# Performance work log

Measured on AMD Instinct MI355X. Metric: run time of the kernel, lower is better.

## Reference

```python
import jax, jax.numpy as jnp
import numpy as np

Z_DIM = 64
K = 2048
N = 32768


def setup_inputs() -> dict:
    key = jax.random.key(0)
    k1, k2 = jax.random.split(key)
    x = jax.random.normal(k1, (N, Z_DIM), dtype=jnp.float32)
    # init.normal_(locs, std=sqrt(z_dim))
    locs = jax.random.normal(k2, (K, Z_DIM), dtype=jnp.float32) * np.sqrt(Z_DIM)
    logits = jnp.zeros((K,), dtype=jnp.float32)  # maxent buffer
    return {"x": x, "locs": locs, "logits": logits}


def reference(x, locs, logits):
    d = x.shape[-1]
    var = jnp.float32(d)  # scale = sqrt(z_dim) -> variance = z_dim
    # squared distances [N, K] via cdist expansion (avoids [N,K,d] intermediate)
    sq = (
        jnp.sum(x * x, axis=-1, keepdims=True)
        + jnp.sum(locs * locs, axis=-1)[None, :]
        - 2.0 * (x @ locs.T)
    )
    # Independent Normal log prob summed over z_dim
    log_norm_const = d * (0.5 * jnp.log(2.0 * jnp.pi) + 0.5 * jnp.log(var))
    comp_log_prob = -0.5 * sq / var - log_norm_const  # [N, K]
    mix_logits = jax.nn.log_softmax(logits)  # Categorical normalizes logits
    wlp = comp_log_prob + mix_logits  # weighted_log_prob, [N, K]
    log_prob = jax.nn.logsumexp(wlp, axis=-1)  # [N]
    modes = jnp.argmax(wlp, axis=-1)  # assign_modes, [N]
    quantized = locs[modes]  # hard_quantize, [N, z_dim]
    return log_prob, quantized
```

## Files before the change

### kernel.cpp

```cpp
#include <hip/hip_runtime.h>
#include <math.h>

#define N_SAMP 32768
#define K_COMP 2048
#define ZD 64
#define LNC 191.896324792608546f
#define LN2F 0.69314718055994531f
#define INV_LN2 1.44269504088896340f
#define S2C 0.02254211001388974f

#define TILES_TOT 128
#define TPS 4
#define STAGES (TILES_TOT / TPS)

typedef __attribute__((ext_vector_type(8))) short short8;
typedef __attribute__((ext_vector_type(4))) float v4f;

#if __has_builtin(__builtin_amdgcn_exp2f)
#define EXP2(x) __builtin_amdgcn_exp2f(x)
#else
#define EXP2(x) exp2f(x)
#endif

typedef const __attribute__((address_space(1))) unsigned int* gas_t;
typedef __attribute__((address_space(3))) unsigned int* las_t;
__device__ inline void gload_lds16(const void* g, void* l) {
    __builtin_amdgcn_global_load_lds((gas_t)g, (las_t)l, 16, 0, 0);
}

__device__ inline unsigned short f2bf(float f) {
    unsigned int u = __float_as_uint(f);
    u += 0x7fffu + ((u >> 16) & 1u);
    return (unsigned short)(u >> 16);
}
__device__ inline float bf2f(unsigned short h) {
    return __uint_as_float(((unsigned int)h) << 16);
}

__global__ __launch_bounds__(256) void prep_kernel(
    const float* __restrict__ locs, const float* __restrict__ logits,
    float* __restrict__ ck2, float* __restrict__ lse_out,
    char* __restrict__ lf) {
    if (blockIdx.x < 32) {
        int gid = blockIdx.x * 256 + threadIdx.x;
        int T = gid >> 6;
        int l = gid & 63;
        int n = l & 15, q = l >> 4;
        int k = T * 16 + n;

        const float* src = locs + (size_t)k * ZD + q * 8;
        float4 u0 = *(const float4*)(src);
        float4 u1 = *(const float4*)(src + 4);
        float4 u2 = *(const float4*)(src + 32);
        float4 u3 = *(const float4*)(src + 36);
        float a[8] = {u0.x, u0.y, u0.z, u0.w, u1.x, u1.y, u1.z, u1.w};
        float b[8] = {u2.x, u2.y, u2.z, u2.w, u3.x, u3.y, u3.z, u3.w};

        short8 h0, h1, l0, l1;
        float sq = 0.f;
#pragma unroll
        for (int j = 0; j < 8; ++j) {
            unsigned short ha = f2bf(a[j]);
            h0[j] = (short)ha; l0[j] = (short)f2bf(a[j] - bf2f(ha));
            unsigned short hb = f2bf(b[j]);
            h1[j] = (short)hb; l1[j] = (short)f2bf(b[j] - bf2f(hb));
            sq = fmaf(a[j], a[j], sq);
            sq = fmaf(b[j], b[j], sq);
        }
        char* dst = lf + (size_t)T * 4096 + l * 16;
        *(short8*)(dst)        = h0;
        *(short8*)(dst + 1024) = h1;
        *(short8*)(dst + 2048) = l0;
        *(short8*)(dst + 3072) = l1;

        sq += __shfl_xor(sq, 16);
        sq += __shfl_xor(sq, 32);
        if (q == 0) ck2[k] = (logits[k] - sq * (1.0f / 128.0f)) * INV_LN2;
    } else {
        __shared__ float red[4];
        int tid = threadIdx.x;
        int wv = tid >> 6, ln = tid & 63;
        float lm = -INFINITY;
        for (int i = tid; i < K_COMP; i += 256) lm = fmaxf(lm, logits[i]);
#pragma unroll
        for (int d = 1; d < 64; d <<= 1) lm = fmaxf(lm, __shfl_xor(lm, d));
        if (ln == 0) red[wv] = lm;
        __syncthreads();
        float M = fmaxf(fmaxf(red[0], red[1]), fmaxf(red[2], red[3]));
        float ls = 0.f;
        for (int i = tid; i < K_COMP; i += 256) ls += __expf(logits[i] - M);
#pragma unroll
        for (int d = 1; d < 64; d <<= 1) ls += __shfl_xor(ls, d);
        __syncthreads();
        if (ln == 0) red[wv] = ls;
        __syncthreads();
        if (tid == 0) *lse_out = M + __logf(red[0] + red[1] + red[2] + red[3]);
    }
}

__global__ __launch_bounds__(256, 2) void mix_kernel(
    const float* __restrict__ x, const float* __restrict__ locs,
    const char* __restrict__ lf, const float* __restrict__ ck2,
    const float* __restrict__ lse_ptr, float* __restrict__ out) {

    __shared__ char buf[2][TPS * 4096];
    __shared__ int amax_sh[64];

    const int tid  = threadIdx.x;
    const int lane = tid & 63;
    const int wv   = __builtin_amdgcn_readfirstlane(tid >> 6);
    const int n    = lane & 15;
    const int quad = lane >> 4;
    const int sbase = blockIdx.x * 64;
    const int srow  = sbase + wv * 16 + n;

    short8 bh0, bh1, bl0, bl1;
    float xs;
    {
        const float* xp = x + (size_t)srow * ZD + quad * 8;
        float4 u0 = *(const float4*)(xp);
        float4 u1 = *(const float4*)(xp + 4);
        float4 u2 = *(const float4*)(xp + 32);
        float4 u3 = *(const float4*)(xp + 36);
        float a[8] = {u0.x, u0.y, u0.z, u0.w, u1.x, u1.y, u1.z, u1.w};
        float b[8] = {u2.x, u2.y, u2.z, u2.w, u3.x, u3.y, u3.z, u3.w};
        float p = 0.f;
#pragma unroll
        for (int j = 0; j < 8; ++j) {
            unsigned short h;
            h = f2bf(a[j]); bh0[j] = (short)h; bl0[j] = (short)f2bf(a[j] - bf2f(h));
            h = f2bf(b[j]); bh1[j] = (short)h; bl1[j] = (short)f2bf(b[j] - bf2f(h));
            p = fmaf(a[j], a[j], p);
            p = fmaf(b[j], b[j], p);
        }
        p += __shfl_xor(p, 16);
        p += __shfl_xor(p, 32);
        xs = p;
    }

    const char* gsrc0 = lf + (size_t)wv * 4096 + lane * 16;
    char* ldst0 = &buf[0][wv * 4096];

#define DMA(S, b) do {                                                   \
    const char* _g = gsrc0 + (size_t)(S) * (TPS * 4096);                 \
    char* _l = ldst0 + (b) * (TPS * 4096);                               \
    gload_lds16(_g, _l);                                                 \
    gload_lds16(_g + 1024, _l + 1024);                                   \
    gload_lds16(_g + 2048, _l + 2048);                                   \
    gload_lds16(_g + 3072, _l + 3072);                                   \
} while (0)

    float mm = -1e30f, s0 = 0.f, s1 = 0.f;
    int ai = 0;

#define EPI(acc, fcv, kb) do {                                                 \
    float w0 = fmaf((acc).x, S2C, (fcv).x);                                    \
    float w1 = fmaf((acc).y, S2C, (fcv).y);                                    \
    float w2 = fmaf((acc).z, S2C, (fcv).z);                                    \
    float w3 = fmaf((acc).w, S2C, (fcv).w);                                    \
    s0 += EXP2(w0) + EXP2(w1);                                                 \
    s1 += EXP2(w2) + EXP2(w3);                                                 \
    float t01 = fmaxf(w0, w1); int i01 = (w1 > w0) ? ((kb) + 1) : ((kb) + 0);  \
    float t23 = fmaxf(w2, w3); int i23 = (w3 > w2) ? ((kb) + 3) : ((kb) + 2);  \
    float tt2 = fmaxf(t01, t23); int it = (t23 > t01) ? i23 : i01;             \
    ai = (tt2 > mm) ? it : ai;                                                 \
    mm = fmaxf(mm, tt2);                                                       \
} while (0)

    DMA(0, 0);
    __syncthreads();

    for (int S = 0; S < STAGES; ++S) {
        const int b = S & 1;
        if (S + 1 < STAGES) DMA(S + 1, b ^ 1);

        const float* ckS = ck2 + S * (TPS * 16) + quad * 4;
        float4 fc0 = *(const float4*)(ckS);
        float4 fc1 = *(const float4*)(ckS + 16);
        float4 fc2 = *(const float4*)(ckS + 32);
        float4 fc3 = *(const float4*)(ckS + 48);

        const char* base = &buf[b][lane * 16];
        const int kb0 = S * (TPS * 16) + quad * 4;

#pragma unroll
        for (int j = 0; j < TPS; j += 2) {
            const char* p0 = base + j * 4096;
            const char* p1 = base + (j + 1) * 4096;
            short8 a00 = *(const short8*)(p0);
            short8 a01 = *(const short8*)(p0 + 1024);
            short8 a02 = *(const short8*)(p0 + 2048);
            short8 a03 = *(const short8*)(p0 + 3072);
            short8 a10 = *(const short8*)(p1);
            short8 a11 = *(const short8*)(p1 + 1024);
            short8 a12 = *(const short8*)(p1 + 2048);
            short8 a13 = *(const short8*)(p1 + 3072);

            v4f ca = {0.f, 0.f, 0.f, 0.f};
            v4f cb = {0.f, 0.f, 0.f, 0.f};
            ca = __builtin_amdgcn_mfma_f32_16x16x32_bf16(a00, bh0, ca, 0, 0, 0);
            cb = __builtin_amdgcn_mfma_f32_16x16x32_bf16(a10, bh0, cb, 0, 0, 0);
            ca = __builtin_amdgcn_mfma_f32_16x16x32_bf16(a01, bh1, ca, 0, 0, 0);
            cb = __builtin_amdgcn_mfma_f32_16x16x32_bf16(a11, bh1, cb, 0, 0, 0);
            ca = __builtin_amdgcn_mfma_f32_16x16x32_bf16(a00, bl0, ca, 0, 0, 0);
            cb = __builtin_amdgcn_mfma_f32_16x16x32_bf16(a10, bl0, cb, 0, 0, 0);
            ca = __builtin_amdgcn_mfma_f32_16x16x32_bf16(a01, bl1, ca, 0, 0, 0);
            cb = __builtin_amdgcn_mfma_f32_16x16x32_bf16(a11, bl1, cb, 0, 0, 0);
            ca = __builtin_amdgcn_mfma_f32_16x16x32_bf16(a02, bh0, ca, 0, 0, 0);
            cb = __builtin_amdgcn_mfma_f32_16x16x32_bf16(a12, bh0, cb, 0, 0, 0);
            ca = __builtin_amdgcn_mfma_f32_16x16x32_bf16(a03, bh1, ca, 0, 0, 0);
            cb = __builtin_amdgcn_mfma_f32_16x16x32_bf16(a13, bh1, cb, 0, 0, 0);

            if (j == 0) { EPI(ca, fc0, kb0 + 0 * 16); EPI(cb, fc1, kb0 + 1 * 16); }
            else        { EPI(ca, fc2, kb0 + 2 * 16); EPI(cb, fc3, kb0 + 3 * 16); }
        }
        __syncthreads();
    }

    float sum = s0 + s1;
#pragma unroll
    for (int d = 16; d <= 32; d <<= 1) {
        sum += __shfl_xor(sum, d);
        float om = __shfl_xor(mm, d);
        int   oa = __shfl_xor(ai, d);
        ai = (om > mm || (om == mm && oa < ai)) ? oa : ai;
        mm = fmaxf(mm, om);
    }

    if (quad == 0) {
        float bias = -xs * (1.0f / 128.0f) - LNC;
        out[srow] = fmaf(__log2f(sum), LN2F, bias - lse_ptr[0]);
        amax_sh[wv * 16 + n] = ai;
    }
    __syncthreads();

    const float4* lq = (const float4*)locs;
    float4* oq = (float4*)(out + N_SAMP + (size_t)sbase * ZD);
#pragma unroll
    for (int i = tid; i < 64 * (ZD / 4); i += 256) {
        int r = i >> 4, c = i & 15;
        oq[i] = lq[(size_t)amax_sh[r] * (ZD / 4) + c];
    }
#undef DMA
#undef EPI
}

extern "C" void kernel_launch(void* const* d_in, const int* in_sizes, int n_in,
                              void* d_out, int out_size, void* d_ws, size_t ws_size,
                              hipStream_t stream) {
    const float* x      = (const float*)d_in[0];
    const float* locs   = (const float*)d_in[1];
    const float* logits = (const float*)d_in[2];
    float* out = (float*)d_out;

    float* ck2 = (float*)d_ws;
    float* lse = ck2 + K_COMP;
    char*  lf  = (char*)d_ws + 16384;

    prep_kernel<<<33, 256, 0, stream>>>(locs, logits, ck2, lse, lf);
    mix_kernel<<<N_SAMP / 64, 256, 0, stream>>>(x, locs, lf, ck2, lse, out);
}
```

Before: 100.4 us.

## Drop low-bf16 locs split, track top-3 candidates and rescore exactly in fp32

The locs operand is now kept only as a single bf16 value, which removes the locs-low terms and cuts the MFMAs per 16-component tile from six to four. It also halves the LDS/global traffic per tile, and the stage size doubles to 8 tiles. Because the lower-precision scores can mis-order near-ties, each row tracks its top-3 groups of four components, and after the loop those 12 candidates are rescored with exact fp32 dot products to choose the argmax. The logsumexp now also uses the reduced-precision dot product, which could loosen accuracy, and the extra top-3 bookkeeping adds work to the inner epilogue.

```diff
diff --git a/kernel.cpp b/kernel.cpp
--- a/kernel.cpp
+++ b/kernel.cpp
@@ -10,8 +10,9 @@
 #define S2C 0.02254211001388974f
 
 #define TILES_TOT 128
-#define TPS 4
+#define TPS 8
 #define STAGES (TILES_TOT / TPS)
+#define STAGE_B (TPS * 2048)
 
 typedef __attribute__((ext_vector_type(8))) short short8;
 typedef __attribute__((ext_vector_type(4))) float v4f;
@@ -36,46 +37,39 @@
 __device__ inline float bf2f(unsigned short h) {
     return __uint_as_float(((unsigned int)h) << 16);
 }
+__device__ inline float med3f(float x, float y, float z) {
+    return fmaxf(fminf(x, y), fminf(fmaxf(x, y), z));
+}
 
 __global__ __launch_bounds__(256) void prep_kernel(
     const float* __restrict__ locs, const float* __restrict__ logits,
     float* __restrict__ ck2, float* __restrict__ lse_out,
     char* __restrict__ lf) {
-    if (blockIdx.x < 32) {
+    if (blockIdx.x < 64) {
         int gid = blockIdx.x * 256 + threadIdx.x;
-        int T = gid >> 6;
-        int l = gid & 63;
-        int n = l & 15, q = l >> 4;
-        int k = T * 16 + n;
-
-        const float* src = locs + (size_t)k * ZD + q * 8;
+        int k = gid >> 3;
+        int dc = gid & 7;
+        int T = k >> 4, n = k & 15;
+
+        const float* src = locs + (size_t)k * ZD + dc * 8;
         float4 u0 = *(const float4*)(src);
         float4 u1 = *(const float4*)(src + 4);
-        float4 u2 = *(const float4*)(src + 32);
-        float4 u3 = *(const float4*)(src + 36);
         float a[8] = {u0.x, u0.y, u0.z, u0.w, u1.x, u1.y, u1.z, u1.w};
-        float b[8] = {u2.x, u2.y, u2.z, u2.w, u3.x, u3.y, u3.z, u3.w};
-
-        short8 h0, h1, l0, l1;
+
+        short8 h;
         float sq = 0.f;
 #pragma unroll
         for (int j = 0; j < 8; ++j) {
-            unsigned short ha = f2bf(a[j]);
-            h0[j] = (short)ha; l0[j] = (short)f2bf(a[j] - bf2f(ha));
-            unsigned short hb = f2bf(b[j]);
-            h1[j] = (short)hb; l1[j] = (short)f2bf(b[j] - bf2f(hb));
+            h[j] = (short)f2bf(a[j]);
             sq = fmaf(a[j], a[j], sq);
-            sq = fmaf(b[j], b[j], sq);
-        }
-        char* dst = lf + (size_t)T * 4096 + l * 16;
-        *(short8*)(dst)        = h0;
-        *(short8*)(dst + 1024) = h1;
-        *(short8*)(dst + 2048) = l0;
-        *(short8*)(dst + 3072) = l1;
-
-        sq += __shfl_xor(sq, 16);
-        sq += __shfl_xor(sq, 32);
-        if (q == 0) ck2[k] = (logits[k] - sq * (1.0f / 128.0f)) * INV_LN2;
+        }
+        *(short8*)(lf + (size_t)T * 2048 + (dc >> 2) * 1024 +
+                   ((size_t)(n + 16 * (dc & 3))) * 16) = h;
+
+        sq += __shfl_xor(sq, 1);
+        sq += __shfl_xor(sq, 2);
+        sq += __shfl_xor(sq, 4);
+        if (dc == 0) ck2[k] = (logits[k] - sq * (1.0f / 128.0f)) * INV_LN2;
     } else {
         __shared__ float red[4];
         int tid = threadIdx.x;
@@ -103,7 +97,8 @@
     const char* __restrict__ lf, const float* __restrict__ ck2,
     const float* __restrict__ lse_ptr, float* __restrict__ out) {
 
-    __shared__ char buf[2][TPS * 4096];
+    __shared__ char buf[2][STAGE_B];
+    __shared__ int cb1[64], cb2[64], cb3[64];
     __shared__ int amax_sh[64];
 
     const int tid  = threadIdx.x;
@@ -142,30 +137,17 @@
     char* ldst0 = &buf[0][wv * 4096];
 
 #define DMA(S, b) do {                                                   \
-    const char* _g = gsrc0 + (size_t)(S) * (TPS * 4096);                 \
-    char* _l = ldst0 + (b) * (TPS * 4096);                               \
+    const char* _g = gsrc0 + (size_t)(S) * STAGE_B;                      \
+    char* _l = ldst0 + (b) * STAGE_B;                                    \
     gload_lds16(_g, _l);                                                 \
     gload_lds16(_g + 1024, _l + 1024);                                   \
     gload_lds16(_g + 2048, _l + 2048);                                   \
     gload_lds16(_g + 3072, _l + 3072);                                   \
 } while (0)
 
-    float mm = -1e30f, s0 = 0.f, s1 = 0.f;
-    int ai = 0;
-
-#define EPI(acc, fcv, kb) do {                                                 \
-    float w0 = fmaf((acc).x, S2C, (fcv).x);                                    \
-    float w1 = fmaf((acc).y, S2C, (fcv).y);                                    \
-    float w2 = fmaf((acc).z, S2C, (fcv).z);                                    \
-    float w3 = fmaf((acc).w, S2C, (fcv).w);                                    \
-    s0 += EXP2(w0) + EXP2(w1);                                                 \
-    s1 += EXP2(w2) + EXP2(w3);                                                 \
-    float t01 = fmaxf(w0, w1); int i01 = (w1 > w0) ? ((kb) + 1) : ((kb) + 0);  \
-    float t23 = fmaxf(w2, w3); int i23 = (w3 > w2) ? ((kb) + 3) : ((kb) + 2);  \
-    float tt2 = fmaxf(t01, t23); int it = (t23 > t01) ? i23 : i01;             \
-    ai = (tt2 > mm) ? it : ai;                                                 \
-    mm = fmaxf(mm, tt2);                                                       \
-} while (0)
+    float m1 = -1e30f, m2 = -1e30f, m3 = -1e30f;
+    int i1 = 0, i2 = 0, i3 = 0;
+    float s0 = 0.f, s1 = 0.f;
 
     DMA(0, 0);
     __syncthreads();
@@ -175,44 +157,42 @@
         if (S + 1 < STAGES) DMA(S + 1, b ^ 1);
 
         const float* ckS = ck2 + S * (TPS * 16) + quad * 4;
-        float4 fc0 = *(const float4*)(ckS);
-        float4 fc1 = *(const float4*)(ckS + 16);
-        float4 fc2 = *(const float4*)(ckS + 32);
-        float4 fc3 = *(const float4*)(ckS + 48);
-
         const char* base = &buf[b][lane * 16];
         const int kb0 = S * (TPS * 16) + quad * 4;
 
 #pragma unroll
-        for (int j = 0; j < TPS; j += 2) {
-            const char* p0 = base + j * 4096;
-            const char* p1 = base + (j + 1) * 4096;
-            short8 a00 = *(const short8*)(p0);
-            short8 a01 = *(const short8*)(p0 + 1024);
-            short8 a02 = *(const short8*)(p0 + 2048);
-            short8 a03 = *(const short8*)(p0 + 3072);
-            short8 a10 = *(const short8*)(p1);
-            short8 a11 = *(const short8*)(p1 + 1024);
-            short8 a12 = *(const short8*)(p1 + 2048);
-            short8 a13 = *(const short8*)(p1 + 3072);
-
-            v4f ca = {0.f, 0.f, 0.f, 0.f};
-            v4f cb = {0.f, 0.f, 0.f, 0.f};
-            ca = __builtin_amdgcn_mfma_f32_16x16x32_bf16(a00, bh0, ca, 0, 0, 0);
-            cb = __builtin_amdgcn_mfma_f32_16x16x32_bf16(a10, bh0, cb, 0, 0, 0);
-            ca = __builtin_amdgcn_mfma_f32_16x16x32_bf16(a01, bh1, ca, 0, 0, 0);
-            cb = __builtin_amdgcn_mfma_f32_16x16x32_bf16(a11, bh1, cb, 0, 0, 0);
-            ca = __builtin_amdgcn_mfma_f32_16x16x32_bf16(a00, bl0, ca, 0, 0, 0);
-            cb = __builtin_amdgcn_mfma_f32_16x16x32_bf16(a10, bl0, cb, 0, 0, 0);
-            ca = __builtin_amdgcn_mfma_f32_16x16x32_bf16(a01, bl1, ca, 0, 0, 0);
-            cb = __builtin_amdgcn_mfma_f32_16x16x32_bf16(a11, bl1, cb, 0, 0, 0);
-            ca = __builtin_amdgcn_mfma_f32_16x16x32_bf16(a02, bh0, ca, 0, 0, 0);
-            cb = __builtin_amdgcn_mfma_f32_16x16x32_bf16(a12, bh0, cb, 0, 0, 0);
-            ca = __builtin_amdgcn_mfma_f32_16x16x32_bf16(a03, bh1, ca, 0, 0, 0);
-            cb = __builtin_amdgcn_mfma_f32_16x16x32_bf16(a13, bh1, cb, 0, 0, 0);
-
-            if (j == 0) { EPI(ca, fc0, kb0 + 0 * 16); EPI(cb, fc1, kb0 + 1 * 16); }
-            else        { EPI(ca, fc2, kb0 + 2 * 16); EPI(cb, fc3, kb0 + 3 * 16); }
+        for (int j = 0; j < TPS; ++j) {
+            const char* p0 = base + j * 2048;
+            short8 a0 = *(const short8*)(p0);
+            short8 a1 = *(const short8*)(p0 + 1024);
+            float4 cc = *(const float4*)(ckS + j * 16);
+
+            v4f acc = {0.f, 0.f, 0.f, 0.f};
+            acc = __builtin_amdgcn_mfma_f32_16x16x32_bf16(a0, bh0, acc, 0, 0, 0);
+            acc = __builtin_amdgcn_mfma_f32_16x16x32_bf16(a1, bh1, acc, 0, 0, 0);
+            acc = __builtin_amdgcn_mfma_f32_16x16x32_bf16(a0, bl0, acc, 0, 0, 0);
+            acc = __builtin_amdgcn_mfma_f32_16x16x32_bf16(a1, bl1, acc, 0, 0, 0);
+
+            const int kb = kb0 + j * 16;
+            float w0 = fmaf(acc.x, S2C, cc.x);
+            float w1 = fmaf(acc.y, S2C, cc.y);
+            float w2 = fmaf(acc.z, S2C, cc.z);
+            float w3 = fmaf(acc.w, S2C, cc.w);
+            s0 += EXP2(w0) + EXP2(w1);
+            s1 += EXP2(w2) + EXP2(w3);
+
+            float T4 = fmaxf(fmaxf(w0, w1), fmaxf(w2, w3));
+            bool c = T4 > m1;
+            float z = fminf(T4, m1);
+            int zi = c ? i1 : kb;
+            m1 = fmaxf(T4, m1);
+            i1 = c ? kb : i1;
+            float m3old = m3;
+            bool c2 = z > m2;
+            m3 = med3f(z, m2, m3);
+            i3 = c2 ? i2 : ((z > m3old) ? zi : i3);
+            m2 = fmaxf(z, m2);
+            i2 = c2 ? zi : i2;
         }
         __syncthreads();
     }
@@ -221,16 +201,61 @@
 #pragma unroll
     for (int d = 16; d <= 32; d <<= 1) {
         sum += __shfl_xor(sum, d);
-        float om = __shfl_xor(mm, d);
-        int   oa = __shfl_xor(ai, d);
-        ai = (om > mm || (om == mm && oa < ai)) ? oa : ai;
-        mm = fmaxf(mm, om);
+        float M1 = __shfl_xor(m1, d), M2 = __shfl_xor(m2, d), M3 = __shfl_xor(m3, d);
+        int   I1 = __shfl_xor(i1, d), I2 = __shfl_xor(i2, d), I3 = __shfl_xor(i3, d);
+        bool cc = (M1 > m1) || (M1 == m1 && I1 < i1);
+        float w2v = cc ? M2 : m2;  int w2i = cc ? I2 : i2;
+        float w3v = cc ? M3 : m3;  int w3i = cc ? I3 : i3;
+        float lv  = cc ? m1 : M1;  int li  = cc ? i1 : I1;
+        float l2v = cc ? m2 : M2;  int l2i = cc ? i2 : I2;
+        m1 = cc ? M1 : m1;  i1 = cc ? I1 : i1;
+        bool c2 = lv > w2v;
+        float nm2 = c2 ? lv : w2v;  int ni2 = c2 ? li : w2i;
+        float z3 = c2 ? w2v : lv;   int zi3 = c2 ? w2i : li;
+        float nm3 = fmaxf(z3, fmaxf(w3v, l2v));
+        int ni3 = (z3 >= w3v && z3 >= l2v) ? zi3 : ((w3v >= l2v) ? w3i : l2i);
+        m2 = nm2; i2 = ni2; m3 = nm3; i3 = ni3;
     }
 
     if (quad == 0) {
         float bias = -xs * (1.0f / 128.0f) - LNC;
         out[srow] = fmaf(__log2f(sum), LN2F, bias - lse_ptr[0]);
-        amax_sh[wv * 16 + n] = ai;
+        int s = wv * 16 + n;
+        cb1[s] = i1; cb2[s] = i2; cb3[s] = i3;
+    }
+    __syncthreads();
+
+    {
+        int s = tid >> 2;
+        int jj = tid & 3;
+        const float4* xrow = (const float4*)(x + (size_t)(sbase + s) * ZD);
+        float bestv = -1e30f;
+        int bestk = 0x7fffffff;
+        int bases[3] = {cb1[s], cb2[s], cb3[s]};
+#pragma unroll
+        for (int ci = 0; ci < 3; ++ci) {
+            int k = bases[ci] + jj;
+            const float4* lrow = (const float4*)(locs + (size_t)k * ZD);
+            float dot = 0.f;
+#pragma unroll
+            for (int dd = 0; dd < 16; ++dd) {
+                float4 xv = xrow[dd];
+                float4 lv = lrow[dd];
+                dot = fmaf(xv.x, lv.x, dot);
+                dot = fmaf(xv.y, lv.y, dot);
+                dot = fmaf(xv.z, lv.z, dot);
+                dot = fmaf(xv.w, lv.w, dot);
+            }
+            float v = fmaf(dot, S2C, ck2[k]);
+            if (v > bestv || (v == bestv && k < bestk)) { bestv = v; bestk = k; }
+        }
+#pragma unroll
+        for (int d = 1; d <= 2; d <<= 1) {
+            float ov = __shfl_xor(bestv, d);
+            int   ok = __shfl_xor(bestk, d);
+            if (ov > bestv || (ov == bestv && ok < bestk)) { bestv = ov; bestk = ok; }
+        }
+        if (jj == 0) amax_sh[s] = bestk;
     }
     __syncthreads();
 
@@ -242,7 +267,6 @@
         oq[i] = lq[(size_t)amax_sh[r] * (ZD / 4) + c];
     }
 #undef DMA
-#undef EPI
 }
 
 extern "C" void kernel_launch(void* const* d_in, const int* in_sizes, int n_in,
@@ -254,9 +278,9 @@
     float* out = (float*)d_out;
 
     float* ck2 = (float*)d_ws;
-    float* lse = ck2 + K_COMP;
+    float* lse = (float*)((char*)d_ws + 8192);
     char*  lf  = (char*)d_ws + 16384;
 
-    prep_kernel<<<33, 256, 0, stream>>>(locs, logits, ck2, lse, lf);
+    prep_kernel<<<65, 256, 0, stream>>>(locs, logits, ck2, lse, lf);
     mix_kernel<<<N_SAMP / 64, 256, 0, stream>>>(x, locs, lf, ck2, lse, out);
 }
```

Result: slower. 118.4 us (+17.9%).
